# Kernel tuning notes

Measured on AMD Instinct MI355X. Metric: run time of the kernel, lower is better.

## Reference

```python
import jax, jax.numpy as jnp
import numpy as np

IN_FF = 7  # joints
MASK = np.ones(9, dtype=np.float32)  # [P(3), RPY sin/cos (6)]


def _mlp(x, params):
    # params: list of (W, b); sigmoid after every layer except the last (predict)
    h = x
    for W, b in params[:-1]:
        h = jax.nn.sigmoid(h @ W + b)
    W, b = params[-1]
    return h @ W + b


def _rpy_head(x, params):
    # FeedForwardNet_RPY forward: y -> [sin(y0), cos(y1)], angle = atan2(sin, cos)
    y = _mlp(x, params)
    s = jnp.sin(y[..., 0])
    c = jnp.cos(y[..., 1])
    ang = jnp.arctan2(s, c)
    return jnp.stack([s, c, ang], axis=-1)  # (..., 3)


def setup_inputs():
    key = jax.random.key(0)
    ks = jax.random.split(key, 26)
    m = 16384
    d = {"x": jax.random.normal(ks[0], (m, 2 * IN_FF), jnp.float32)}

    def lin(k, fi, fo, name, i):
        k1, k2 = jax.random.split(k)
        lim = 1.0 / np.sqrt(fi)  # torch Linear default init
        d[name + "_W" + str(i)] = jax.random.uniform(k1, (fi, fo), jnp.float32, -lim, lim)
        d[name + "_b" + str(i)] = jax.random.uniform(k2, (fo,), jnp.float32, -lim, lim)

    idx = 1
    for name, dims in [("pos", [7, 512, 512, 3]), ("roll", [7, 256, 256, 2]),
                       ("pitch", [7, 256, 256, 2]), ("yaw", [7, 256, 256, 2])]:
        for i in range(3):
            lin(ks[idx], dims[i], dims[i + 1], name, i)
            idx += 1
    return d


def _forward(x, pos_p, roll_p, pitch_p, yaw_p):
    mask = jnp.asarray(MASK)
    M_P, M_RPY = mask[:3], mask[3:]
    q, qdot = x[:, :IN_FF], x[:, IN_FF:]

    # position net: forward + per-sample Jacobian (exact, replaces the autograd loop)
    P = _mlp(q, pos_p)                                          # (m, 3)
    J_P = jax.vmap(jax.jacfwd(lambda z: _mlp(z, pos_p)))(q)     # (m, 3, 7)
    vel = jnp.einsum("moi,mi->mo", J_P, qdot)                   # bmm(J_P, jointVels)
    P = P * M_P
    vel = vel * M_P

    heads = []
    for p in (roll_p, pitch_p, yaw_p):
        f = lambda z, p=p: _rpy_head(z, p)
        y = f(q)                                # (m, 3): [sin, cos, angle]
        J = jax.vmap(jax.jacfwd(f))(q)          # (m, 3, 7)
        v = jnp.einsum("moi,mi->mo", J[:, :2, :], qdot)  # (m, 2)
        heads.append((y, J, v))
    (yR, JR, vR), (yPi, JPi, vPi), (yY, JY, vY) = heads

    # order: [roll_sin, pitch_sin, yaw_sin, roll_cos, pitch_cos, yaw_cos]
    RPY = jnp.stack([yR[:, 0], yPi[:, 0], yY[:, 0], yR[:, 1], yPi[:, 1], yY[:, 1]], axis=1) * M_RPY
    vel_RPY = jnp.stack([vR[:, 0], vPi[:, 0], vY[:, 0], vR[:, 1], vPi[:, 1], vY[:, 1]], axis=1) * M_RPY
    J_RPY = jnp.stack([JR[:, 0], JPi[:, 0], JY[:, 0], JR[:, 1], JPi[:, 1], JY[:, 1]], axis=1)  # (m,6,7)

    out = jnp.concatenate([P, RPY, vel, vel_RPY], axis=1)            # (m, 18)
    J_tot = jnp.concatenate([J_P, J_RPY], axis=1)                    # (m, 9, 7)
    out_angles = jnp.concatenate([P, yR[:, 2:3], yPi[:, 2:3], yY[:, 2:3]], axis=1)       # (m, 6)
    J_tot_angles = jnp.concatenate([J_P, JR[:, 2:3], JPi[:, 2:3], JY[:, 2:3]], axis=1)   # (m, 6, 7)
    return out, J_tot, out_angles, J_tot_angles


def reference(x, pos_W0, pos_b0, pos_W1, pos_b1, pos_W2, pos_b2,
              roll_W0, roll_b0, roll_W1, roll_b1, roll_W2, roll_b2,
              pitch_W0, pitch_b0, pitch_W1, pitch_b1, pitch_W2, pitch_b2,
              yaw_W0, yaw_b0, yaw_W1, yaw_b1, yaw_W2, yaw_b2):
    pos_p = [(pos_W0, pos_b0), (pos_W1, pos_b1), (pos_W2, pos_b2)]
    roll_p = [(roll_W0, roll_b0), (roll_W1, roll_b1), (roll_W2, roll_b2)]
    pitch_p = [(pitch_W0, pitch_b0), (pitch_W1, pitch_b1), (pitch_W2, pitch_b2)]
    yaw_p = [(yaw_W0, yaw_b0), (yaw_W1, yaw_b1), (yaw_W2, yaw_b2)]
    return _forward(x, pos_p, roll_p, pitch_p, yaw_p)
```

## Files before the change

kernel.cpp:

```cpp
#include <hip/hip_runtime.h>
#include <math.h>

typedef __attribute__((ext_vector_type(8))) short short8;
typedef __attribute__((ext_vector_type(4))) float floatx4;

__device__ __forceinline__ float sig(float z) { return 1.0f / (1.0f + __expf(-z)); }

__device__ __forceinline__ unsigned short f2bf(float f) {
    unsigned u = __float_as_uint(f);
    u = (u + 0x7FFFu + ((u >> 16) & 1u)) >> 16;
    return (unsigned short)u;
}

__device__ __forceinline__ unsigned int pack2bf(float a, float b) {
    unsigned ua = __float_as_uint(a), ub = __float_as_uint(b);
    ua += 0x7FFFu + ((ua >> 16) & 1u);
    ub += 0x7FFFu + ((ub >> 16) & 1u);
    return __builtin_amdgcn_perm(ub, ua, 0x07060302);
}

__global__ void convert_all(const float* __restrict__ s0, const float* __restrict__ s1,
                            const float* __restrict__ s2, const float* __restrict__ s3,
                            unsigned short* __restrict__ ws) {
    int idx = blockIdx.x * 256 + threadIdx.x;
    const float* src; unsigned short* dst; int H, logH, local;
    if (idx < 262144) { src = s0; dst = ws; H = 512; logH = 9; local = idx; }
    else {
        int r = idx - 262144; int m = r >> 16; local = r & 65535;
        H = 256; logH = 8;
        src = (m == 0) ? s1 : (m == 1) ? s2 : s3;
        dst = ws + 262144 + m * 65536;
    }
    int n = local & (H - 1), k = local >> logH;
    int KT = H >> 5;
    int blk = (n >> 4) * KT + (k >> 5);
    int lane = ((k >> 3) & 3) * 16 + (n & 15);
    int j = k & 7;
    dst[(blk * 64 + lane) * 8 + j] = f2bf(src[local]);
}

struct PosS { float B0[512], B1[512], W2[1536], Q[4][8], Qd[4][8]; };
struct RpyS { float B0[256], B1[256], W2[512],  Q[8][8], Qd[8][8]; };

__global__ __launch_bounds__(256, 3)
void fused_mfma(const float* __restrict__ x,
                const float* __restrict__ pW0, const float* __restrict__ pb0,
                const float* __restrict__ pb1,
                const float* __restrict__ pW2, const float* __restrict__ pb2,
                const float* __restrict__ rW0_, const float* __restrict__ rb0_,
                const float* __restrict__ rb1_,
                const float* __restrict__ rW2_, const float* __restrict__ rb2_,
                const float* __restrict__ piW0, const float* __restrict__ pib0,
                const float* __restrict__ pib1,
                const float* __restrict__ piW2, const float* __restrict__ pib2,
                const float* __restrict__ yW0, const float* __restrict__ yb0,
                const float* __restrict__ yb1,
                const float* __restrict__ yW2, const float* __restrict__ yb2,
                const unsigned short* __restrict__ wsBase,
                float* __restrict__ out, int ns)
{
    extern __shared__ unsigned short sA[];
    float* dynF = (float*)sA;
    __shared__ union { PosS p; RpyS r; } sU;

    const int tid = threadIdx.x;
    const int f = blockIdx.x;
    const int g = f / 5, r5 = f % 5;
    const size_t JTOT = (size_t)ns * 18, OUTA = (size_t)ns * 81, JANG = (size_t)ns * 87;
    const floatx4 z4 = {0.f, 0.f, 0.f, 0.f};
    const int w = tid >> 6, lane = tid & 63;
    const int quad = lane >> 4, col = lane & 15;
    const int srcl = lane & 47;

    if (r5 < 2) {
        const int m0 = (g * 2 + r5) * 4;

        for (int i = tid; i < 512;  i += 256) { sU.p.B0[i] = pb0[i]; sU.p.B1[i] = pb1[i]; }
        for (int i = tid; i < 1536; i += 256) sU.p.W2[i] = pW2[i];
        if (tid < 56) {
            int m = tid / 14, c = tid % 14;
            float v = x[(m0 + m) * 14 + c];
            if (c < 7) sU.p.Q[m][c] = v; else sU.p.Qd[m][c - 7] = v;
        }
        __syncthreads();

        const float4* W04 = (const float4*)pW0;
        #pragma unroll
        for (int t = 0; t < 2; ++t) {
            int item = tid + t * 256;
            int s = item >> 7, gg = item & 127;
            int kt = gg >> 3, kq = (gg >> 1) & 3, j0 = (gg & 1) * 4;
            int sw = kt & 7;
            int k = gg * 4;
            float q[7]; float4 w0r[7];
            #pragma unroll
            for (int i = 0; i < 7; i++) { q[i] = sU.p.Q[s][i]; w0r[i] = W04[i * 128 + gg]; }
            float hv[4], dv[4];
            #pragma unroll
            for (int jj = 0; jj < 4; jj++) {
                float z = sU.p.B0[k + jj];
                #pragma unroll
                for (int i = 0; i < 7; i++) z = fmaf(q[i], ((const float*)&w0r[i])[jj], z);
                float hh = sig(z);
                hv[jj] = hh; dv[jj] = hh - hh * hh;
            }
            const int rt = s >> 1, rb = (s & 1) * 8;
            {
                int cl = (kq * 16 + rb) ^ sw;
                uint2 v; v.x = pack2bf(hv[0], hv[1]); v.y = pack2bf(hv[2], hv[3]);
                *(uint2*)&sA[(rt * 16 + kt) * 512 + cl * 8 + j0] = v;
            }
            #pragma unroll
            for (int i = 0; i < 7; i++) {
                int cl = (kq * 16 + rb + 1 + i) ^ sw;
                uint2 v;
                v.x = pack2bf(dv[0] * ((const float*)&w0r[i])[0], dv[1] * ((const float*)&w0r[i])[1]);
                v.y = pack2bf(dv[2] * ((const float*)&w0r[i])[2], dv[3] * ((const float*)&w0r[i])[3]);
                *(uint2*)&sA[(rt * 16 + kt) * 512 + cl * 8 + j0] = v;
            }
        }
        __syncthreads();

        floatx4 acc[2][8];
        #pragma unroll
        for (int rt = 0; rt < 2; rt++)
            #pragma unroll
            for (int ct = 0; ct < 8; ct++) acc[rt][ct] = z4;

        const short8* bbase = (const short8*)wsBase + (size_t)(w * 128) * 64 + lane;
        #pragma unroll
        for (int kt = 0; kt < 16; ++kt) {
            const int sw = kt & 7;
            short8 bf[8];
            #pragma unroll
            for (int ct = 0; ct < 8; ++ct) bf[ct] = bbase[(ct * 16 + kt) * 64];
            short8 a0 = *(const short8*)&sA[(kt) * 512 + (lane ^ sw) * 8];
            short8 a1 = *(const short8*)&sA[(16 + kt) * 512 + (lane ^ sw) * 8];
            #pragma unroll
            for (int ct = 0; ct < 8; ++ct) {
                acc[0][ct] = __builtin_amdgcn_mfma_f32_16x16x32_bf16(a0, bf[ct], acc[0][ct], 0, 0, 0);
                acc[1][ct] = __builtin_amdgcn_mfma_f32_16x16x32_bf16(a1, bf[ct], acc[1][ct], 0, 0, 0);
            }
        }

        float ep[2][4][3];
        #pragma unroll
        for (int a = 0; a < 2; a++) for (int b = 0; b < 4; b++) for (int c = 0; c < 3; c++) ep[a][b][c] = 0.f;
        #pragma unroll
        for (int ct = 0; ct < 8; ++ct) {
            const int n = w * 128 + ct * 16 + col;
            const float b1n = sU.p.B1[n];
            const float w20 = sU.p.W2[n * 3], w21 = sU.p.W2[n * 3 + 1], w22 = sU.p.W2[n * 3 + 2];
            #pragma unroll
            for (int rt = 0; rt < 2; ++rt) {
                float z2c = __shfl(acc[rt][ct][0], srcl);
                float h2 = sig(z2c + b1n);
                float d2 = h2 - h2 * h2;
                #pragma unroll
                for (int r = 0; r < 4; ++r) {
                    float gg = ((quad & 1) == 0 && r == 0) ? h2 : d2 * acc[rt][ct][r];
                    ep[rt][r][0] = fmaf(gg, w20, ep[rt][r][0]);
                    ep[rt][r][1] = fmaf(gg, w21, ep[rt][r][1]);
                    ep[rt][r][2] = fmaf(gg, w22, ep[rt][r][2]);
                }
            }
        }
        #pragma unroll
        for (int mask = 1; mask <= 8; mask <<= 1)
            #pragma unroll
            for (int a = 0; a < 2; a++)
                #pragma unroll
                for (int b = 0; b < 4; b++)
                    #pragma unroll
                    for (int c = 0; c < 3; c++)
                        ep[a][b][c] += __shfl_xor(ep[a][b][c], mask);
        __syncthreads();
        if (col == 0) {
            #pragma unroll
            for (int rt = 0; rt < 2; ++rt)
                #pragma unroll
                for (int r = 0; r < 4; ++r) {
                    int row = rt * 16 + quad * 4 + r;
                    dynF[(w * 32 + row) * 3 + 0] = ep[rt][r][0];
                    dynF[(w * 32 + row) * 3 + 1] = ep[rt][r][1];
                    dynF[(w * 32 + row) * 3 + 2] = ep[rt][r][2];
                }
        }
        __syncthreads();
        if (tid < 96) {
            int row = tid / 3, j = tid % 3;
            float v = dynF[row * 3 + j] + dynF[(32 + row) * 3 + j]
                    + dynF[(64 + row) * 3 + j] + dynF[(96 + row) * 3 + j];
            int i_row = row & 7, s = row >> 3;
            size_t M = m0 + s;
            if (i_row == 0) { v += pb2[j]; out[M * 18 + j] = v; out[OUTA + M * 6 + j] = v; }
            else            { out[JTOT + M * 63 + j * 7 + (i_row - 1)] = v;
                              out[JANG + M * 42 + j * 7 + (i_row - 1)] = v; }
            dynF[384 + row * 3 + j] = v;
        }
        __syncthreads();
        if (tid < 12) {
            int s = tid / 3, j = tid % 3;
            float vel = 0.f;
            #pragma unroll
            for (int i = 0; i < 7; i++)
                vel = fmaf(dynF[384 + (s * 8 + 1 + i) * 3 + j], sU.p.Qd[s][i], vel);
            out[(size_t)(m0 + s) * 18 + 9 + j] = vel;
        }
    } else {
        const int h = r5 - 2;
        const int m0 = g * 8;
        const float* W0 = (h == 0) ? rW0_ : (h == 1) ? piW0 : yW0;
        const float* b0 = (h == 0) ? rb0_ : (h == 1) ? pib0 : yb0;
        const float* b1 = (h == 0) ? rb1_ : (h == 1) ? pib1 : yb1;
        const float* W2 = (h == 0) ? rW2_ : (h == 1) ? piW2 : yW2;
        const float* b2 = (h == 0) ? rb2_ : (h == 1) ? pib2 : yb2;
        const unsigned short* wsW1 = wsBase + 262144 + h * 65536;

        if (tid < 256) { sU.r.B0[tid] = b0[tid]; sU.r.B1[tid] = b1[tid]; }
        for (int i = tid; i < 512; i += 256) sU.r.W2[i] = W2[i];
        if (tid < 112) {
            int m = tid / 14, c = tid % 14;
            float v = x[(m0 + m) * 14 + c];
            if (c < 7) sU.r.Q[m][c] = v; else sU.r.Qd[m][c - 7] = v;
        }
        __syncthreads();

        const float4* W04 = (const float4*)W0;
        #pragma unroll
        for (int t = 0; t < 2; ++t) {
            int item = tid + t * 256;
            int s = item >> 6, gg = item & 63;
            int kt = gg >> 3, kq = (gg >> 1) & 3, j0 = (gg & 1) * 4;
            int sw = kt & 7;
            int k = gg * 4;
            float q[7]; float4 w0r[7];
            #pragma unroll
            for (int i = 0; i < 7; i++) { q[i] = sU.r.Q[s][i]; w0r[i] = W04[i * 64 + gg]; }
            float hv[4], dv[4];
            #pragma unroll
            for (int jj = 0; jj < 4; jj++) {
                float z = sU.r.B0[k + jj];
                #pragma unroll
                for (int i = 0; i < 7; i++) z = fmaf(q[i], ((const float*)&w0r[i])[jj], z);
                float hh = sig(z);
                hv[jj] = hh; dv[jj] = hh - hh * hh;
            }
            const int rt = s >> 1, rb = (s & 1) * 8;
            {
                int cl = (kq * 16 + rb) ^ sw;
                uint2 v; v.x = pack2bf(hv[0], hv[1]); v.y = pack2bf(hv[2], hv[3]);
                *(uint2*)&sA[(rt * 8 + kt) * 512 + cl * 8 + j0] = v;
            }
            #pragma unroll
            for (int i = 0; i < 7; i++) {
                int cl = (kq * 16 + rb + 1 + i) ^ sw;
                uint2 v;
                v.x = pack2bf(dv[0] * ((const float*)&w0r[i])[0], dv[1] * ((const float*)&w0r[i])[1]);
                v.y = pack2bf(dv[2] * ((const float*)&w0r[i])[2], dv[3] * ((const float*)&w0r[i])[3]);
                *(uint2*)&sA[(rt * 8 + kt) * 512 + cl * 8 + j0] = v;
            }
        }
        __syncthreads();

        floatx4 acc[4][4];
        #pragma unroll
        for (int rt = 0; rt < 4; rt++)
            #pragma unroll
            for (int ct = 0; ct < 4; ct++) acc[rt][ct] = z4;

        const short8* bbase = (const short8*)wsW1 + (size_t)(w * 32) * 64 + lane;
        #pragma unroll
        for (int kt = 0; kt < 8; ++kt) {
            const int sw = kt & 7;
            short8 bf[4];
            #pragma unroll
            for (int ct = 0; ct < 4; ++ct) bf[ct] = bbase[(ct * 8 + kt) * 64];
            short8 afr[4];
            #pragma unroll
            for (int rt = 0; rt < 4; ++rt)
                afr[rt] = *(const short8*)&sA[(rt * 8 + kt) * 512 + (lane ^ sw) * 8];
            #pragma unroll
            for (int ct = 0; ct < 4; ++ct)
                #pragma unroll
                for (int rt = 0; rt < 4; ++rt)
                    acc[rt][ct] = __builtin_amdgcn_mfma_f32_16x16x32_bf16(afr[rt], bf[ct], acc[rt][ct], 0, 0, 0);
        }

        float ep[4][4][2];
        #pragma unroll
        for (int a = 0; a < 4; a++) for (int b = 0; b < 4; b++) for (int c = 0; c < 2; c++) ep[a][b][c] = 0.f;
        #pragma unroll
        for (int ct = 0; ct < 4; ++ct) {
            const int n = w * 64 + ct * 16 + col;
            const float b1n = sU.r.B1[n];
            const float w20 = sU.r.W2[n * 2], w21 = sU.r.W2[n * 2 + 1];
            #pragma unroll
            for (int rt = 0; rt < 4; ++rt) {
                float z2c = __shfl(acc[rt][ct][0], srcl);
                float h2 = sig(z2c + b1n);
                float d2 = h2 - h2 * h2;
                #pragma unroll
                for (int r = 0; r < 4; ++r) {
                    float gg = ((quad & 1) == 0 && r == 0) ? h2 : d2 * acc[rt][ct][r];
                    ep[rt][r][0] = fmaf(gg, w20, ep[rt][r][0]);
                    ep[rt][r][1] = fmaf(gg, w21, ep[rt][r][1]);
                }
            }
        }
        #pragma unroll
        for (int mask = 1; mask <= 8; mask <<= 1)
            #pragma unroll
            for (int a = 0; a < 4; a++)
                #pragma unroll
                for (int b = 0; b < 4; b++)
                    #pragma unroll
                    for (int c = 0; c < 2; c++)
                        ep[a][b][c] += __shfl_xor(ep[a][b][c], mask);
        __syncthreads();
        if (col == 0) {
            #pragma unroll
            for (int rt = 0; rt < 4; ++rt)
                #pragma unroll
                for (int r = 0; r < 4; ++r) {
                    int row = rt * 16 + quad * 4 + r;
                    dynF[(w * 64 + row) * 2 + 0] = ep[rt][r][0];
                    dynF[(w * 64 + row) * 2 + 1] = ep[rt][r][1];
                }
        }
        __syncthreads();
        if (tid < 128) {
            int row = tid >> 1, j = tid & 1;
            float v = dynF[row * 2 + j] + dynF[(64 + row) * 2 + j]
                    + dynF[(128 + row) * 2 + j] + dynF[(192 + row) * 2 + j];
            if ((row & 7) == 0) v += b2[j];
            dynF[512 + row * 2 + j] = v;
        }
        __syncthreads();
        if (tid < 8) {
            int s = tid;
            size_t M = m0 + s;
            float y0 = dynF[512 + (s * 8) * 2 + 0], y1 = dynF[512 + (s * 8) * 2 + 1];
            float sv = sinf(y0), cv = cosf(y1);
            out[M * 18 + 3 + h] = sv;
            out[M * 18 + 6 + h] = cv;
            out[OUTA + M * 6 + 3 + h] = atan2f(sv, cv);
            float f0 = cosf(y0), f1 = -sinf(y1);
            float inv = 1.0f / fmaf(sv, sv, cv * cv);
            float v0 = 0.f, v1 = 0.f;
            #pragma unroll
            for (int i = 0; i < 7; i++) {
                float r0 = f0 * dynF[512 + (s * 8 + 1 + i) * 2 + 0];
                float r1 = f1 * dynF[512 + (s * 8 + 1 + i) * 2 + 1];
                out[JTOT + M * 63 + (3 + h) * 7 + i] = r0;
                out[JTOT + M * 63 + (6 + h) * 7 + i] = r1;
                out[JANG + M * 42 + (3 + h) * 7 + i] = (cv * r0 - sv * r1) * inv;
                v0 = fmaf(r0, sU.r.Qd[s][i], v0);
                v1 = fmaf(r1, sU.r.Qd[s][i], v1);
            }
            out[M * 18 + 12 + h] = v0;
            out[M * 18 + 15 + h] = v1;
        }
    }
}

extern "C" void kernel_launch(void* const* d_in, const int* in_sizes, int n_in,
                              void* d_out, int out_size, void* d_ws, size_t ws_size,
                              hipStream_t stream) {
    (void)n_in; (void)out_size; (void)ws_size;
    const float* x = (const float*)d_in[0];
    float* out = (float*)d_out;
    unsigned short* ws = (unsigned short*)d_ws;
    const int ns = in_sizes[0] / 14;

    convert_all<<<dim3(1792), 256, 0, stream>>>(
        (const float*)d_in[3], (const float*)d_in[9],
        (const float*)d_in[15], (const float*)d_in[21], ws);

    fused_mfma<<<dim3((ns / 8) * 5), 256, 32768, stream>>>(
        x,
        (const float*)d_in[1],  (const float*)d_in[2],  (const float*)d_in[4],
        (const float*)d_in[5],  (const float*)d_in[6],
        (const float*)d_in[7],  (const float*)d_in[8],  (const float*)d_in[10],
        (const float*)d_in[11], (const float*)d_in[12],
        (const float*)d_in[13], (const float*)d_in[14], (const float*)d_in[16],
        (const float*)d_in[17], (const float*)d_in[18],
        (const float*)d_in[19], (const float*)d_in[20], (const float*)d_in[22],
        (const float*)d_in[23], (const float*)d_in[24],
        ws, out, ns);
}
```

Baseline: 349.6 us.

## Make fused MLP-Jacobian kernel loop over multiple sample tiles per block

The fused kernel now gives each block a loop over several 4- or 8-sample tiles: pos blocks handle 32 samples and RPY blocks handle a strided set of head/sample tiles. Biases and output weights are loaded into LDS once per block instead of once per tile, and the next tile's inputs are prefetched into a triple-buffered slot during the MFMA phase. It also swaps sigmoid's divide for a hardware reciprocal and uses a packed bf16 convert builtin when one is available. The cost is fewer blocks, which may leave CUs idle or unbalanced, plus more static LDS and slightly lower reciprocal precision.

```diff
diff --git a/kernel.cpp b/kernel.cpp
--- a/kernel.cpp
+++ b/kernel.cpp
@@ -4,7 +4,9 @@
 typedef __attribute__((ext_vector_type(8))) short short8;
 typedef __attribute__((ext_vector_type(4))) float floatx4;
 
-__device__ __forceinline__ float sig(float z) { return 1.0f / (1.0f + __expf(-z)); }
+__device__ __forceinline__ float sig(float z) {
+    return __builtin_amdgcn_rcpf(1.0f + __expf(-z));
+}
 
 __device__ __forceinline__ unsigned short f2bf(float f) {
     unsigned u = __float_as_uint(f);
@@ -12,12 +14,20 @@
     return (unsigned short)u;
 }
 
+#if __has_builtin(__builtin_amdgcn_cvt_pk_bf16_f32)
+typedef __attribute__((ext_vector_type(2))) short short2v;
+__device__ __forceinline__ unsigned int pack2bf(float a, float b) {
+    short2v r = __builtin_amdgcn_cvt_pk_bf16_f32(a, b);
+    return *(unsigned int*)&r;
+}
+#else
 __device__ __forceinline__ unsigned int pack2bf(float a, float b) {
     unsigned ua = __float_as_uint(a), ub = __float_as_uint(b);
     ua += 0x7FFFu + ((ua >> 16) & 1u);
     ub += 0x7FFFu + ((ub >> 16) & 1u);
     return __builtin_amdgcn_perm(ub, ua, 0x07060302);
 }
+#endif
 
 __global__ void convert_all(const float* __restrict__ s0, const float* __restrict__ s1,
                             const float* __restrict__ s2, const float* __restrict__ s3,
@@ -39,327 +49,345 @@
     dst[(blk * 64 + lane) * 8 + j] = f2bf(src[local]);
 }
 
-struct PosS { float B0[512], B1[512], W2[1536], Q[4][8], Qd[4][8]; };
-struct RpyS { float B0[256], B1[256], W2[512],  Q[8][8], Qd[8][8]; };
-
 __global__ __launch_bounds__(256, 3)
-void fused_mfma(const float* __restrict__ x,
-                const float* __restrict__ pW0, const float* __restrict__ pb0,
-                const float* __restrict__ pb1,
-                const float* __restrict__ pW2, const float* __restrict__ pb2,
-                const float* __restrict__ rW0_, const float* __restrict__ rb0_,
-                const float* __restrict__ rb1_,
-                const float* __restrict__ rW2_, const float* __restrict__ rb2_,
-                const float* __restrict__ piW0, const float* __restrict__ pib0,
-                const float* __restrict__ pib1,
-                const float* __restrict__ piW2, const float* __restrict__ pib2,
-                const float* __restrict__ yW0, const float* __restrict__ yb0,
-                const float* __restrict__ yb1,
-                const float* __restrict__ yW2, const float* __restrict__ yb2,
-                const unsigned short* __restrict__ wsBase,
-                float* __restrict__ out, int ns)
+void fused_persist(const float* __restrict__ x,
+                   const float* __restrict__ pW0, const float* __restrict__ pb0,
+                   const float* __restrict__ pb1,
+                   const float* __restrict__ pW2, const float* __restrict__ pb2,
+                   const float* __restrict__ rW0_, const float* __restrict__ rb0_,
+                   const float* __restrict__ rb1_,
+                   const float* __restrict__ rW2_, const float* __restrict__ rb2_,
+                   const float* __restrict__ piW0, const float* __restrict__ pib0,
+                   const float* __restrict__ pib1,
+                   const float* __restrict__ piW2, const float* __restrict__ pib2,
+                   const float* __restrict__ yW0, const float* __restrict__ yb0,
+                   const float* __restrict__ yb1,
+                   const float* __restrict__ yW2, const float* __restrict__ yb2,
+                   const unsigned short* __restrict__ wsBase,
+                   float* __restrict__ out, int ns)
 {
     extern __shared__ unsigned short sA[];
-    float* dynF = (float*)sA;
-    __shared__ union { PosS p; RpyS r; } sU;
+    __shared__ float sB0[512], sB1[512], sW2[1536];
+    __shared__ float sQx[3][8][16];
+    __shared__ float sScr[4][64][3];
+    __shared__ float sSum[2][64][3];
 
     const int tid = threadIdx.x;
-    const int f = blockIdx.x;
-    const int g = f / 5, r5 = f % 5;
+    const int w = tid >> 6, lane = tid & 63;
+    const int quad = lane >> 4, col = lane & 15, srcl = lane & 47;
     const size_t JTOT = (size_t)ns * 18, OUTA = (size_t)ns * 81, JANG = (size_t)ns * 87;
     const floatx4 z4 = {0.f, 0.f, 0.f, 0.f};
-    const int w = tid >> 6, lane = tid & 63;
-    const int quad = lane >> 4, col = lane & 15;
-    const int srcl = lane & 47;
-
-    if (r5 < 2) {
-        const int m0 = (g * 2 + r5) * 4;
-
-        for (int i = tid; i < 512;  i += 256) { sU.p.B0[i] = pb0[i]; sU.p.B1[i] = pb1[i]; }
-        for (int i = tid; i < 1536; i += 256) sU.p.W2[i] = pW2[i];
+
+    if ((blockIdx.x & 1) == 0) {
+        const int pid = blockIdx.x >> 1;
+        if (tid < 128) {
+            ((float4*)sB0)[tid] = ((const float4*)pb0)[tid];
+            ((float4*)sB1)[tid] = ((const float4*)pb1)[tid];
+        }
+        for (int j = tid; j < 384; j += 256) ((float4*)sW2)[j] = ((const float4*)pW2)[j];
         if (tid < 56) {
             int m = tid / 14, c = tid % 14;
-            float v = x[(m0 + m) * 14 + c];
-            if (c < 7) sU.p.Q[m][c] = v; else sU.p.Qd[m][c - 7] = v;
+            sQx[0][m][c] = x[((size_t)pid * 32 + m) * 14 + c];
         }
         __syncthreads();
 
         const float4* W04 = (const float4*)pW0;
-        #pragma unroll
-        for (int t = 0; t < 2; ++t) {
-            int item = tid + t * 256;
-            int s = item >> 7, gg = item & 127;
-            int kt = gg >> 3, kq = (gg >> 1) & 3, j0 = (gg & 1) * 4;
-            int sw = kt & 7;
-            int k = gg * 4;
-            float q[7]; float4 w0r[7];
-            #pragma unroll
-            for (int i = 0; i < 7; i++) { q[i] = sU.p.Q[s][i]; w0r[i] = W04[i * 128 + gg]; }
-            float hv[4], dv[4];
-            #pragma unroll
-            for (int jj = 0; jj < 4; jj++) {
-                float z = sU.p.B0[k + jj];
-                #pragma unroll
-                for (int i = 0; i < 7; i++) z = fmaf(q[i], ((const float*)&w0r[i])[jj], z);
-                float hh = sig(z);
-                hv[jj] = hh; dv[jj] = hh - hh * hh;
-            }
-            const int rt = s >> 1, rb = (s & 1) * 8;
-            {
-                int cl = (kq * 16 + rb) ^ sw;
-                uint2 v; v.x = pack2bf(hv[0], hv[1]); v.y = pack2bf(hv[2], hv[3]);
-                *(uint2*)&sA[(rt * 16 + kt) * 512 + cl * 8 + j0] = v;
-            }
-            #pragma unroll
-            for (int i = 0; i < 7; i++) {
-                int cl = (kq * 16 + rb + 1 + i) ^ sw;
-                uint2 v;
-                v.x = pack2bf(dv[0] * ((const float*)&w0r[i])[0], dv[1] * ((const float*)&w0r[i])[1]);
-                v.y = pack2bf(dv[2] * ((const float*)&w0r[i])[2], dv[3] * ((const float*)&w0r[i])[3]);
-                *(uint2*)&sA[(rt * 16 + kt) * 512 + cl * 8 + j0] = v;
-            }
-        }
-        __syncthreads();
-
-        floatx4 acc[2][8];
-        #pragma unroll
-        for (int rt = 0; rt < 2; rt++)
-            #pragma unroll
-            for (int ct = 0; ct < 8; ct++) acc[rt][ct] = z4;
-
-        const short8* bbase = (const short8*)wsBase + (size_t)(w * 128) * 64 + lane;
-        #pragma unroll
-        for (int kt = 0; kt < 16; ++kt) {
-            const int sw = kt & 7;
-            short8 bf[8];
-            #pragma unroll
-            for (int ct = 0; ct < 8; ++ct) bf[ct] = bbase[(ct * 16 + kt) * 64];
-            short8 a0 = *(const short8*)&sA[(kt) * 512 + (lane ^ sw) * 8];
-            short8 a1 = *(const short8*)&sA[(16 + kt) * 512 + (lane ^ sw) * 8];
+        for (int k = 0; k < 8; ++k) {
+            const int m0 = pid * 32 + k * 4;
+            const int slot = k % 3;
+            #pragma unroll
+            for (int t = 0; t < 2; ++t) {
+                int item = tid + t * 256;
+                int s = item >> 7, gg = item & 127;
+                int kt = gg >> 3, kq = (gg >> 1) & 3, j0 = (gg & 1) * 4;
+                int sw = kt & 7;
+                int kk = gg * 4;
+                float q[7]; float4 w0r[7];
+                #pragma unroll
+                for (int i = 0; i < 7; i++) { q[i] = sQx[slot][s][i]; w0r[i] = W04[i * 128 + gg]; }
+                float hv[4], dv[4];
+                #pragma unroll
+                for (int jj = 0; jj < 4; jj++) {
+                    float z = sB0[kk + jj];
+                    #pragma unroll
+                    for (int i = 0; i < 7; i++) z = fmaf(q[i], ((const float*)&w0r[i])[jj], z);
+                    float hh = sig(z);
+                    hv[jj] = hh; dv[jj] = hh - hh * hh;
+                }
+                const int rt = s >> 1, rb = (s & 1) * 8;
+                {
+                    int cl = (kq * 16 + rb) ^ sw;
+                    uint2 v; v.x = pack2bf(hv[0], hv[1]); v.y = pack2bf(hv[2], hv[3]);
+                    *(uint2*)&sA[(rt * 16 + kt) * 512 + cl * 8 + j0] = v;
+                }
+                #pragma unroll
+                for (int i = 0; i < 7; i++) {
+                    int cl = (kq * 16 + rb + 1 + i) ^ sw;
+                    uint2 v;
+                    v.x = pack2bf(dv[0] * ((const float*)&w0r[i])[0], dv[1] * ((const float*)&w0r[i])[1]);
+                    v.y = pack2bf(dv[2] * ((const float*)&w0r[i])[2], dv[3] * ((const float*)&w0r[i])[3]);
+                    *(uint2*)&sA[(rt * 16 + kt) * 512 + cl * 8 + j0] = v;
+                }
+            }
+            __syncthreads();
+            if (k + 1 < 8 && tid < 56) {
+                int m = tid / 14, c = tid % 14;
+                sQx[(k + 1) % 3][m][c] = x[((size_t)m0 + 4 + m) * 14 + c];
+            }
+            floatx4 acc[2][8];
+            #pragma unroll
+            for (int rt = 0; rt < 2; rt++)
+                #pragma unroll
+                for (int ct = 0; ct < 8; ct++) acc[rt][ct] = z4;
+            const short8* bbase = (const short8*)wsBase + (size_t)(w * 128) * 64 + lane;
+            #pragma unroll
+            for (int kt = 0; kt < 16; ++kt) {
+                const int sw = kt & 7;
+                short8 bf[8];
+                #pragma unroll
+                for (int ct = 0; ct < 8; ++ct) bf[ct] = bbase[(ct * 16 + kt) * 64];
+                short8 a0 = *(const short8*)&sA[kt * 512 + (lane ^ sw) * 8];
+                short8 a1 = *(const short8*)&sA[(16 + kt) * 512 + (lane ^ sw) * 8];
+                #pragma unroll
+                for (int ct = 0; ct < 8; ++ct) {
+                    acc[0][ct] = __builtin_amdgcn_mfma_f32_16x16x32_bf16(a0, bf[ct], acc[0][ct], 0, 0, 0);
+                    acc[1][ct] = __builtin_amdgcn_mfma_f32_16x16x32_bf16(a1, bf[ct], acc[1][ct], 0, 0, 0);
+                }
+            }
+            float ep[2][4][3];
+            #pragma unroll
+            for (int a = 0; a < 2; a++) for (int b = 0; b < 4; b++) for (int c = 0; c < 3; c++) ep[a][b][c] = 0.f;
             #pragma unroll
             for (int ct = 0; ct < 8; ++ct) {
-                acc[0][ct] = __builtin_amdgcn_mfma_f32_16x16x32_bf16(a0, bf[ct], acc[0][ct], 0, 0, 0);
-                acc[1][ct] = __builtin_amdgcn_mfma_f32_16x16x32_bf16(a1, bf[ct], acc[1][ct], 0, 0, 0);
-            }
-        }
-
-        float ep[2][4][3];
-        #pragma unroll
-        for (int a = 0; a < 2; a++) for (int b = 0; b < 4; b++) for (int c = 0; c < 3; c++) ep[a][b][c] = 0.f;
-        #pragma unroll
-        for (int ct = 0; ct < 8; ++ct) {
-            const int n = w * 128 + ct * 16 + col;
-            const float b1n = sU.p.B1[n];
-            const float w20 = sU.p.W2[n * 3], w21 = sU.p.W2[n * 3 + 1], w22 = sU.p.W2[n * 3 + 2];
-            #pragma unroll
-            for (int rt = 0; rt < 2; ++rt) {
-                float z2c = __shfl(acc[rt][ct][0], srcl);
-                float h2 = sig(z2c + b1n);
-                float d2 = h2 - h2 * h2;
-                #pragma unroll
-                for (int r = 0; r < 4; ++r) {
-                    float gg = ((quad & 1) == 0 && r == 0) ? h2 : d2 * acc[rt][ct][r];
-                    ep[rt][r][0] = fmaf(gg, w20, ep[rt][r][0]);
-                    ep[rt][r][1] = fmaf(gg, w21, ep[rt][r][1]);
-                    ep[rt][r][2] = fmaf(gg, w22, ep[rt][r][2]);
-                }
-            }
-        }
-        #pragma unroll
-        for (int mask = 1; mask <= 8; mask <<= 1)
-            #pragma unroll
-            for (int a = 0; a < 2; a++)
-                #pragma unroll
-                for (int b = 0; b < 4; b++)
-                    #pragma unroll
-                    for (int c = 0; c < 3; c++)
-                        ep[a][b][c] += __shfl_xor(ep[a][b][c], mask);
-        __syncthreads();
-        if (col == 0) {
-            #pragma unroll
-            for (int rt = 0; rt < 2; ++rt)
-                #pragma unroll
-                for (int r = 0; r < 4; ++r) {
-                    int row = rt * 16 + quad * 4 + r;
-                    dynF[(w * 32 + row) * 3 + 0] = ep[rt][r][0];
-                    dynF[(w * 32 + row) * 3 + 1] = ep[rt][r][1];
-                    dynF[(w * 32 + row) * 3 + 2] = ep[rt][r][2];
-                }
-        }
-        __syncthreads();
-        if (tid < 96) {
-            int row = tid / 3, j = tid % 3;
-            float v = dynF[row * 3 + j] + dynF[(32 + row) * 3 + j]
-                    + dynF[(64 + row) * 3 + j] + dynF[(96 + row) * 3 + j];
-            int i_row = row & 7, s = row >> 3;
-            size_t M = m0 + s;
-            if (i_row == 0) { v += pb2[j]; out[M * 18 + j] = v; out[OUTA + M * 6 + j] = v; }
-            else            { out[JTOT + M * 63 + j * 7 + (i_row - 1)] = v;
-                              out[JANG + M * 42 + j * 7 + (i_row - 1)] = v; }
-            dynF[384 + row * 3 + j] = v;
-        }
-        __syncthreads();
-        if (tid < 12) {
-            int s = tid / 3, j = tid % 3;
-            float vel = 0.f;
-            #pragma unroll
-            for (int i = 0; i < 7; i++)
-                vel = fmaf(dynF[384 + (s * 8 + 1 + i) * 3 + j], sU.p.Qd[s][i], vel);
-            out[(size_t)(m0 + s) * 18 + 9 + j] = vel;
+                const int n = w * 128 + ct * 16 + col;
+                const float b1n = sB1[n];
+                const float w20 = sW2[n * 3], w21 = sW2[n * 3 + 1], w22 = sW2[n * 3 + 2];
+                #pragma unroll
+                for (int rt = 0; rt < 2; ++rt) {
+                    float z2c = __shfl(acc[rt][ct][0], srcl);
+                    float h2 = sig(z2c + b1n);
+                    float d2 = h2 - h2 * h2;
+                    #pragma unroll
+                    for (int r = 0; r < 4; ++r) {
+                        float gg2 = ((quad & 1) == 0 && r == 0) ? h2 : d2 * acc[rt][ct][r];
+                        ep[rt][r][0] = fmaf(gg2, w20, ep[rt][r][0]);
+                        ep[rt][r][1] = fmaf(gg2, w21, ep[rt][r][1]);
+                        ep[rt][r][2] = fmaf(gg2, w22, ep[rt][r][2]);
+                    }
+                }
+            }
+            #pragma unroll
+            for (int mask = 1; mask <= 8; mask <<= 1)
+                #pragma unroll
+                for (int a = 0; a < 2; a++)
+                    #pragma unroll
+                    for (int b = 0; b < 4; b++)
+                        #pragma unroll
+                        for (int c = 0; c < 3; c++)
+                            ep[a][b][c] += __shfl_xor(ep[a][b][c], mask);
+            if (col == 0) {
+                #pragma unroll
+                for (int rt = 0; rt < 2; ++rt)
+                    #pragma unroll
+                    for (int r = 0; r < 4; ++r) {
+                        int row = rt * 16 + quad * 4 + r;
+                        sScr[w][row][0] = ep[rt][r][0];
+                        sScr[w][row][1] = ep[rt][r][1];
+                        sScr[w][row][2] = ep[rt][r][2];
+                    }
+            }
+            __syncthreads();
+            if (tid < 96) {
+                int row = tid / 3, j = tid % 3;
+                float v = sScr[0][row][j] + sScr[1][row][j] + sScr[2][row][j] + sScr[3][row][j];
+                int i_row = row & 7, s = row >> 3;
+                size_t M = m0 + s;
+                if (i_row == 0) { v += pb2[j]; out[M * 18 + j] = v; out[OUTA + M * 6 + j] = v; }
+                else            { out[JTOT + M * 63 + j * 7 + (i_row - 1)] = v;
+                                  out[JANG + M * 42 + j * 7 + (i_row - 1)] = v; }
+                sSum[k & 1][row][j] = v;
+            }
+            __syncthreads();
+            if (tid < 12) {
+                int s = tid / 3, j = tid % 3;
+                float vel = 0.f;
+                #pragma unroll
+                for (int i = 0; i < 7; i++)
+                    vel = fmaf(sSum[k & 1][s * 8 + 1 + i][j], sQx[slot][s][7 + i], vel);
+                out[(size_t)(m0 + s) * 18 + 9 + j] = vel;
+            }
         }
     } else {
-        const int h = r5 - 2;
-        const int m0 = g * 8;
-        const float* W0 = (h == 0) ? rW0_ : (h == 1) ? piW0 : yW0;
-        const float* b0 = (h == 0) ? rb0_ : (h == 1) ? pib0 : yb0;
-        const float* b1 = (h == 0) ? rb1_ : (h == 1) ? pib1 : yb1;
-        const float* W2 = (h == 0) ? rW2_ : (h == 1) ? piW2 : yW2;
-        const float* b2 = (h == 0) ? rb2_ : (h == 1) ? pib2 : yb2;
-        const unsigned short* wsW1 = wsBase + 262144 + h * 65536;
-
-        if (tid < 256) { sU.r.B0[tid] = b0[tid]; sU.r.B1[tid] = b1[tid]; }
-        for (int i = tid; i < 512; i += 256) sU.r.W2[i] = W2[i];
-        if (tid < 112) {
-            int m = tid / 14, c = tid % 14;
-            float v = x[(m0 + m) * 14 + c];
-            if (c < 7) sU.r.Q[m][c] = v; else sU.r.Qd[m][c - 7] = v;
+        const int rid = blockIdx.x >> 1;
+        int hcur = -1;
+        const float* W0h = rW0_; const float* b1h = rb1_;
+        const float* W2h = rW2_; const float* b2h = rb2_; const float* b0h = rb0_;
+        const unsigned short* wsW1 = wsBase + 262144;
+        {
+            int t0 = rid * 12;
+            int m00 = (t0 & 2047) * 8;
+            if (tid < 112) {
+                int m = tid / 14, c = tid % 14;
+                sQx[0][m][c] = x[((size_t)m00 + m) * 14 + c];
+            }
         }
-        __syncthreads();
-
-        const float4* W04 = (const float4*)W0;
-        #pragma unroll
-        for (int t = 0; t < 2; ++t) {
-            int item = tid + t * 256;
-            int s = item >> 6, gg = item & 63;
-            int kt = gg >> 3, kq = (gg >> 1) & 3, j0 = (gg & 1) * 4;
-            int sw = kt & 7;
-            int k = gg * 4;
-            float q[7]; float4 w0r[7];
-            #pragma unroll
-            for (int i = 0; i < 7; i++) { q[i] = sU.r.Q[s][i]; w0r[i] = W04[i * 64 + gg]; }
-            float hv[4], dv[4];
-            #pragma unroll
-            for (int jj = 0; jj < 4; jj++) {
-                float z = sU.r.B0[k + jj];
-                #pragma unroll
-                for (int i = 0; i < 7; i++) z = fmaf(q[i], ((const float*)&w0r[i])[jj], z);
-                float hh = sig(z);
-                hv[jj] = hh; dv[jj] = hh - hh * hh;
-            }
-            const int rt = s >> 1, rb = (s & 1) * 8;
-            {
-                int cl = (kq * 16 + rb) ^ sw;
-                uint2 v; v.x = pack2bf(hv[0], hv[1]); v.y = pack2bf(hv[2], hv[3]);
-                *(uint2*)&sA[(rt * 8 + kt) * 512 + cl * 8 + j0] = v;
-            }
-            #pragma unroll
-            for (int i = 0; i < 7; i++) {
-                int cl = (kq * 16 + rb + 1 + i) ^ sw;
-                uint2 v;
-                v.x = pack2bf(dv[0] * ((const float*)&w0r[i])[0], dv[1] * ((const float*)&w0r[i])[1]);
-                v.y = pack2bf(dv[2] * ((const float*)&w0r[i])[2], dv[3] * ((const float*)&w0r[i])[3]);
-                *(uint2*)&sA[(rt * 8 + kt) * 512 + cl * 8 + j0] = v;
-            }
-        }
-        __syncthreads();
-
-        floatx4 acc[4][4];
-        #pragma unroll
-        for (int rt = 0; rt < 4; rt++)
-            #pragma unroll
-            for (int ct = 0; ct < 4; ct++) acc[rt][ct] = z4;
-
-        const short8* bbase = (const short8*)wsW1 + (size_t)(w * 32) * 64 + lane;
-        #pragma unroll
-        for (int kt = 0; kt < 8; ++kt) {
-            const int sw = kt & 7;
-            short8 bf[4];
-            #pragma unroll
-            for (int ct = 0; ct < 4; ++ct) bf[ct] = bbase[(ct * 8 + kt) * 64];
-            short8 afr[4];
-            #pragma unroll
-            for (int rt = 0; rt < 4; ++rt)
-                afr[rt] = *(const short8*)&sA[(rt * 8 + kt) * 512 + (lane ^ sw) * 8];
-            #pragma unroll
-            for (int ct = 0; ct < 4; ++ct)
+        for (int k = 0; k < 12; ++k) {
+            const int t = rid * 12 + k;
+            const int h = t >> 11;
+            const int m0 = (t & 2047) * 8;
+            const int slot = k % 3;
+            if (h != hcur) {
+                W0h = (h == 0) ? rW0_ : (h == 1) ? piW0 : yW0;
+                b0h = (h == 0) ? rb0_ : (h == 1) ? pib0 : yb0;
+                b1h = (h == 0) ? rb1_ : (h == 1) ? pib1 : yb1;
+                W2h = (h == 0) ? rW2_ : (h == 1) ? piW2 : yW2;
+                b2h = (h == 0) ? rb2_ : (h == 1) ? pib2 : yb2;
+                wsW1 = wsBase + 262144 + h * 65536;
+                __syncthreads();
+                if (tid < 64) {
+                    ((float4*)sB0)[tid] = ((const float4*)b0h)[tid];
+                    ((float4*)sB1)[tid] = ((const float4*)b1h)[tid];
+                } else if (tid < 192) {
+                    ((float4*)sW2)[tid - 64] = ((const float4*)W2h)[tid - 64];
+                }
+                hcur = h;
+                __syncthreads();
+            }
+            const float4* W04 = (const float4*)W0h;
+            #pragma unroll
+            for (int tt = 0; tt < 2; ++tt) {
+                int item = tid + tt * 256;
+                int s = item >> 6, gg = item & 63;
+                int kt = gg >> 3, kq = (gg >> 1) & 3, j0 = (gg & 1) * 4;
+                int sw = kt & 7;
+                int kk = gg * 4;
+                float q[7]; float4 w0r[7];
+                #pragma unroll
+                for (int i = 0; i < 7; i++) { q[i] = sQx[slot][s][i]; w0r[i] = W04[i * 64 + gg]; }
+                float hv[4], dv[4];
+                #pragma unroll
+                for (int jj = 0; jj < 4; jj++) {
+                    float z = sB0[kk + jj];
+                    #pragma unroll
+                    for (int i = 0; i < 7; i++) z = fmaf(q[i], ((const float*)&w0r[i])[jj], z);
+                    float hh = sig(z);
+                    hv[jj] = hh; dv[jj] = hh - hh * hh;
+                }
+                const int rt = s >> 1, rb = (s & 1) * 8;
+                {
+                    int cl = (kq * 16 + rb) ^ sw;
+                    uint2 v; v.x = pack2bf(hv[0], hv[1]); v.y = pack2bf(hv[2], hv[3]);
+                    *(uint2*)&sA[(rt * 8 + kt) * 512 + cl * 8 + j0] = v;
+                }
+                #pragma unroll
+                for (int i = 0; i < 7; i++) {
+                    int cl = (kq * 16 + rb + 1 + i) ^ sw;
+                    uint2 v;
+                    v.x = pack2bf(dv[0] * ((const float*)&w0r[i])[0], dv[1] * ((const float*)&w0r[i])[1]);
+                    v.y = pack2bf(dv[2] * ((const float*)&w0r[i])[2], dv[3] * ((const float*)&w0r[i])[3]);
+                    *(uint2*)&sA[(rt * 8 + kt) * 512 + cl * 8 + j0] = v;
+                }
+            }
+            __syncthreads();
+            if (k + 1 < 12 && tid < 112) {
+                int t2 = t + 1;
+                int m = tid / 14, c = tid % 14;
+                sQx[(k + 1) % 3][m][c] = x[((size_t)((t2 & 2047) * 8) + m) * 14 + c];
+            }
+            floatx4 acc[4][4];
+            #pragma unroll
+            for (int rt = 0; rt < 4; rt++)
+                #pragma unroll
+                for (int ct = 0; ct < 4; ct++) acc[rt][ct] = z4;
+            const short8* bbase = (const short8*)wsW1 + (size_t)(w * 32) * 64 + lane;
+            #pragma unroll
+            for (int kt = 0; kt < 8; ++kt) {
+                const int sw = kt & 7;
+                short8 bf[4];
+                #pragma unroll
+                for (int ct = 0; ct < 4; ++ct) bf[ct] = bbase[(ct * 8 + kt) * 64];
+                short8 afr[4];
                 #pragma unroll
                 for (int rt = 0; rt < 4; ++rt)
-                    acc[rt][ct] = __builtin_amdgcn_mfma_f32_16x16x32_bf16(afr[rt], bf[ct], acc[rt][ct], 0, 0, 0);
-        }
-
-        float ep[4][4][2];
-        #pragma unroll
-        for (int a = 0; a < 4; a++) for (int b = 0; b < 4; b++) for (int c = 0; c < 2; c++) ep[a][b][c] = 0.f;
-        #pragma unroll
-        for (int ct = 0; ct < 4; ++ct) {
-            const int n = w * 64 + ct * 16 + col;
-            const float b1n = sU.r.B1[n];
-            const float w20 = sU.r.W2[n * 2], w21 = sU.r.W2[n * 2 + 1];
-            #pragma unroll
-            for (int rt = 0; rt < 4; ++rt) {
-                float z2c = __shfl(acc[rt][ct][0], srcl);
-                float h2 = sig(z2c + b1n);
-                float d2 = h2 - h2 * h2;
-                #pragma unroll
-                for (int r = 0; r < 4; ++r) {
-                    float gg = ((quad & 1) == 0 && r == 0) ? h2 : d2 * acc[rt][ct][r];
-                    ep[rt][r][0] = fmaf(gg, w20, ep[rt][r][0]);
-                    ep[rt][r][1] = fmaf(gg, w21, ep[rt][r][1]);
-                }
-            }
-        }
-        #pragma unroll
-        for (int mask = 1; mask <= 8; mask <<= 1)
-            #pragma unroll
-            for (int a = 0; a < 4; a++)
-                #pragma unroll
-                for (int b = 0; b < 4; b++)
-                    #pragma unroll
-                    for (int c = 0; c < 2; c++)
-                        ep[a][b][c] += __shfl_xor(ep[a][b][c], mask);
-        __syncthreads();
-        if (col == 0) {
-            #pragma unroll
-            for (int rt = 0; rt < 4; ++rt)
-                #pragma unroll
-                for (int r = 0; r < 4; ++r) {
-                    int row = rt * 16 + quad * 4 + r;
-                    dynF[(w * 64 + row) * 2 + 0] = ep[rt][r][0];
-                    dynF[(w * 64 + row) * 2 + 1] = ep[rt][r][1];
-                }
-        }
-        __syncthreads();
-        if (tid < 128) {
-            int row = tid >> 1, j = tid & 1;
-            float v = dynF[row * 2 + j] + dynF[(64 + row) * 2 + j]
-                    + dynF[(128 + row) * 2 + j] + dynF[(192 + row) * 2 + j];
-            if ((row & 7) == 0) v += b2[j];
-            dynF[512 + row * 2 + j] = v;
-        }
-        __syncthreads();
-        if (tid < 8) {
-            int s = tid;
-            size_t M = m0 + s;
-            float y0 = dynF[512 + (s * 8) * 2 + 0], y1 = dynF[512 + (s * 8) * 2 + 1];
-            float sv = sinf(y0), cv = cosf(y1);
-            out[M * 18 + 3 + h] = sv;
-            out[M * 18 + 6 + h] = cv;
-            out[OUTA + M * 6 + 3 + h] = atan2f(sv, cv);
-            float f0 = cosf(y0), f1 = -sinf(y1);
-            float inv = 1.0f / fmaf(sv, sv, cv * cv);
-            float v0 = 0.f, v1 = 0.f;
-            #pragma unroll
-            for (int i = 0; i < 7; i++) {
-                float r0 = f0 * dynF[512 + (s * 8 + 1 + i) * 2 + 0];
-                float r1 = f1 * dynF[512 + (s * 8 + 1 + i) * 2 + 1];
-                out[JTOT + M * 63 + (3 + h) * 7 + i] = r0;
-                out[JTOT + M * 63 + (6 + h) * 7 + i] = r1;
-                out[JANG + M * 42 + (3 + h) * 7 + i] = (cv * r0 - sv * r1) * inv;
-                v0 = fmaf(r0, sU.r.Qd[s][i], v0);
-                v1 = fmaf(r1, sU.r.Qd[s][i], v1);
-            }
-            out[M * 18 + 12 + h] = v0;
-            out[M * 18 + 15 + h] = v1;
+                    afr[rt] = *(const short8*)&sA[(rt * 8 + kt) * 512 + (lane ^ sw) * 8];
+                #pragma unroll
+                for (int ct = 0; ct < 4; ++ct)
+                    #pragma unroll
+                    for (int rt = 0; rt < 4; ++rt)
+                        acc[rt][ct] = __builtin_amdgcn_mfma_f32_16x16x32_bf16(afr[rt], bf[ct], acc[rt][ct], 0, 0, 0);
+            }
+            float ep[4][4][2];
+            #pragma unroll
+            for (int a = 0; a < 4; a++) for (int b = 0; b < 4; b++) for (int c = 0; c < 2; c++) ep[a][b][c] = 0.f;
+            #pragma unroll
+            for (int ct = 0; ct < 4; ++ct) {
+                const int n = w * 64 + ct * 16 + col;
+                const float b1n = sB1[n];
+                const float w20 = sW2[n * 2], w21 = sW2[n * 2 + 1];
+                #pragma unroll
+                for (int rt = 0; rt < 4; ++rt) {
+                    float z2c = __shfl(acc[rt][ct][0], srcl);
+                    float h2 = sig(z2c + b1n);
+                    float d2 = h2 - h2 * h2;
+                    #pragma unroll
+                    for (int r = 0; r < 4; ++r) {
+                        float gg2 = ((quad & 1) == 0 && r == 0) ? h2 : d2 * acc[rt][ct][r];
+                        ep[rt][r][0] = fmaf(gg2, w20, ep[rt][r][0]);
+                        ep[rt][r][1] = fmaf(gg2, w21, ep[rt][r][1]);
+                    }
+                }
+            }
+            #pragma unroll
+            for (int mask = 1; mask <= 8; mask <<= 1)
+                #pragma unroll
+                for (int a = 0; a < 4; a++)
+                    #pragma unroll
+                    for (int b = 0; b < 4; b++)
+                        #pragma unroll
+                        for (int c = 0; c < 2; c++)
+                            ep[a][b][c] += __shfl_xor(ep[a][b][c], mask);
+            if (col == 0) {
+                #pragma unroll
+                for (int rt = 0; rt < 4; ++rt)
+                    #pragma unroll
+                    for (int r = 0; r < 4; ++r) {
+                        int row = rt * 16 + quad * 4 + r;
+                        sScr[w][row][0] = ep[rt][r][0];
+                        sScr[w][row][1] = ep[rt][r][1];
+                    }
+            }
+            __syncthreads();
+            if (tid < 128) {
+                int row = tid >> 1, j = tid & 1;
+                float v = sScr[0][row][j] + sScr[1][row][j] + sScr[2][row][j] + sScr[3][row][j];
+                if ((row & 7) == 0) v += b2h[j];
+                sSum[k & 1][row][j] = v;
+            }
+            __syncthreads();
+            if (tid < 8) {
+                int s = tid;
+                size_t M = m0 + s;
+                float y0 = sSum[k & 1][s * 8][0], y1 = sSum[k & 1][s * 8][1];
+                float sv = sinf(y0), cv = cosf(y1);
+                out[M * 18 + 3 + h] = sv;
+                out[M * 18 + 6 + h] = cv;
+                out[OUTA + M * 6 + 3 + h] = atan2f(sv, cv);
+                float f0 = cosf(y0), f1 = -sinf(y1);
+                float inv = __builtin_amdgcn_rcpf(fmaf(sv, sv, cv * cv));
+                float v0 = 0.f, v1 = 0.f;
+                #pragma unroll
+                for (int i = 0; i < 7; i++) {
+                    float r0 = f0 * sSum[k & 1][s * 8 + 1 + i][0];
+                    float r1 = f1 * sSum[k & 1][s * 8 + 1 + i][1];
+                    out[JTOT + M * 63 + (3 + h) * 7 + i] = r0;
+                    out[JTOT + M * 63 + (6 + h) * 7 + i] = r1;
+                    out[JANG + M * 42 + (3 + h) * 7 + i] = (cv * r0 - sv * r1) * inv;
+                    v0 = fmaf(r0, sQx[slot][s][7 + i], v0);
+                    v1 = fmaf(r1, sQx[slot][s][7 + i], v1);
+                }
+                out[M * 18 + 12 + h] = v0;
+                out[M * 18 + 15 + h] = v1;
+            }
         }
     }
 }
@@ -377,7 +405,7 @@
         (const float*)d_in[3], (const float*)d_in[9],
         (const float*)d_in[15], (const float*)d_in[21], ws);
 
-    fused_mfma<<<dim3((ns / 8) * 5), 256, 32768, stream>>>(
+    fused_persist<<<dim3((ns / 32) * 2), 256, 32768, stream>>>(
         x,
         (const float*)d_in[1],  (const float*)d_in[2],  (const float*)d_in[4],
         (const float*)d_in[5],  (const float*)d_in[6],
```

After: 849.0 us. 2.43x slower.
